# Performance work log

Hardware: AMD Instinct MI355X
Metric: run time of the kernel (lower is better)

The kernel has to match this reference:

```python
import jax, jax.numpy as jnp
import numpy as np

DIM = 256
TIME_DIM = 64
BETA = 0.5
VOCAB = 150
B, L = 2048, 128


def setup_inputs() -> dict:
    key = jax.random.key(0)
    ks = jax.random.split(key, 9)
    u = lambda k, shape: jax.random.uniform(k, shape, jnp.float32, -0.1, 0.1)
    return {
        "out": jax.random.normal(ks[0], (B, L, DIM), jnp.float32),
        "hn": jax.random.normal(ks[1], (B, DIM), jnp.float32),
        "pos_ind": jax.random.randint(ks[2], (B, L), 0, VOCAB),
        "rel_dt": jax.random.randint(ks[3], (B, L), 0, VOCAB),
        "abs_dt": jnp.zeros((B, L), jnp.float32),
        "pos_emb_w": u(ks[4], (VOCAB, TIME_DIM)),
        "rel_emb_w": u(ks[5], (VOCAB, TIME_DIM)),
        "Wk": u(ks[6], (DIM, DIM)),   # fc_k.weight: y = x @ Wk.T
        "Wq": u(ks[7], (DIM, DIM)),   # fc_q.weight
        "Wrp": u(ks[8], (1, 2 * TIME_DIM)),  # fc_rp.weight
    }


def reference(out, hn, pos_ind, rel_dt, abs_dt, pos_emb_w, rel_emb_w, Wk, Wq, Wrp):
    temperature = np.sqrt(DIM * 1.0).astype(np.float32)
    pad_mask = pos_ind == 0                      # [B, L]
    pos_e = pos_emb_w[pos_ind]                   # [B, L, T]
    rel_e = rel_emb_w[rel_dt]                    # [B, L, T]
    attn_k = jnp.einsum('bld,ed->ble', out, Wk)  # fc_k(out)
    attn_q = jnp.einsum('bd,ed->be', hn, Wq)     # fc_q(hn)
    attn_0 = jnp.einsum('bld,bd->bl', attn_k, attn_q) / temperature
    attn_1 = jnp.einsum('blt,ot->bl', jnp.concatenate([rel_e, pos_e], -1), Wrp)
    attn = attn_0 + BETA * attn_1
    attn = jnp.where(pad_mask, -jnp.inf, attn)
    attn = jax.nn.softmax(attn, axis=1)
    return jnp.einsum('bl,bld->bd', attn, out)   # [B, D]
```

## Files before the change

kernel.cpp:

```cpp
#include <hip/hip_runtime.h>

#define DIM 256
#define L_ 128
#define TD 64
#define NVOCAB 150
#define NB 2048

__device__ __forceinline__ float dot4(float4 a, float4 b) {
    return fmaf(a.x, b.x, fmaf(a.y, b.y, fmaf(a.z, b.z, a.w * b.w)));
}

__global__ __launch_bounds__(256) void prep_kernel(
    const float* __restrict__ Wk, const float* __restrict__ Wq,
    const float* __restrict__ Wrp,
    const float* __restrict__ rel_emb_w, const float* __restrict__ pos_emb_w,
    float* __restrict__ M, float* __restrict__ rel_s, float* __restrict__ pos_s)
{
    if (blockIdx.x == DIM) {
        int v = threadIdx.x;
        if (v < NVOCAB) {
            float sr = 0.f, sp = 0.f;
#pragma unroll 8
            for (int j = 0; j < TD; ++j) {
                sr = fmaf(rel_emb_w[v * TD + j], Wrp[j], sr);
                sp = fmaf(pos_emb_w[v * TD + j], Wrp[TD + j], sp);
            }
            rel_s[v] = 0.5f * sr;
            pos_s[v] = 0.5f * sp;
        }
        return;
    }
    int cc = blockIdx.x;
    int d  = threadIdx.x;
    float a0 = 0.f, a1 = 0.f, a2 = 0.f, a3 = 0.f;
#pragma unroll 8
    for (int e = 0; e < DIM; e += 4) {
        a0 = fmaf(Wq[(e + 0) * DIM + cc], Wk[(e + 0) * DIM + d], a0);
        a1 = fmaf(Wq[(e + 1) * DIM + cc], Wk[(e + 1) * DIM + d], a1);
        a2 = fmaf(Wq[(e + 2) * DIM + cc], Wk[(e + 2) * DIM + d], a2);
        a3 = fmaf(Wq[(e + 3) * DIM + cc], Wk[(e + 3) * DIM + d], a3);
    }
    M[cc * DIM + d] = (a0 + a1 + a2 + a3) * (1.0f / 16.0f);
}

__global__ __launch_bounds__(256) void qk_bias_kernel(
    const float* __restrict__ hn, const float* __restrict__ M,
    const int* __restrict__ pos_ind, const int* __restrict__ rel_dt,
    const float* __restrict__ rel_s, const float* __restrict__ pos_s,
    float* __restrict__ qk, float* __restrict__ bias_g)
{
    const int t = threadIdx.x;
    if (blockIdx.x >= NB / 8) {
        int idx = (blockIdx.x - NB / 8) * 256 + t;
        int pi = pos_ind[idx];
        int rd = rel_dt[idx];
        bias_g[idx] = (pi == 0) ? -1e30f : (rel_s[rd] + pos_s[pi]);
        return;
    }
    __shared__ float hn_s[8][DIM];
    const int r0 = blockIdx.x * 8;
#pragma unroll
    for (int i = 0; i < 8; ++i)
        hn_s[i][t] = hn[(size_t)(r0 + i) * DIM + t];
    __syncthreads();
    float acc[8] = {0.f, 0.f, 0.f, 0.f, 0.f, 0.f, 0.f, 0.f};
#pragma unroll 8
    for (int c = 0; c < DIM; ++c) {
        float m = M[c * DIM + t];
#pragma unroll
        for (int r = 0; r < 8; ++r)
            acc[r] = fmaf(hn_s[r][c], m, acc[r]);
    }
#pragma unroll
    for (int r = 0; r < 8; ++r)
        qk[(size_t)(r0 + r) * DIM + t] = acc[r];
}

__global__ __launch_bounds__(256) void attn_wave(
    const float* __restrict__ outp, const float* __restrict__ qk,
    const float* __restrict__ bias_g, float* __restrict__ y)
{
    const int w    = threadIdx.x >> 6;
    const int lane = threadIdx.x & 63;
    const int g    = lane >> 4;
    const int c    = lane & 15;
    const int b    = (blockIdx.x << 2) | w;

    const float4* __restrict__ src = (const float4*)outp + (size_t)b * (L_ * 64);
    const float4* __restrict__ qp  = (const float4*)qk + (size_t)b * 64;
    const float*  __restrict__ bp  = bias_g + (size_t)b * L_;

    float4 q[4];
#pragma unroll
    for (int j = 0; j < 4; ++j) q[j] = qp[j * 16 + c];

    float4 o[4];
#pragma unroll
    for (int j = 0; j < 4; ++j) o[j] = make_float4(0.f, 0.f, 0.f, 0.f);
    float d = 0.f;

    float4 va[4], vb[4];
    float biA, biB;

#define LOADV(BUF, ROW)                                            \
    do {                                                           \
        _Pragma("unroll")                                          \
        for (int j = 0; j < 4; ++j)                                \
            BUF[j] = src[(ROW) * 64 + j * 16 + c];                 \
    } while (0)

#define PROC(BUF, BI)                                              \
    do {                                                           \
        float p = dot4(BUF[0], q[0]) + dot4(BUF[1], q[1]) +        \
                  dot4(BUF[2], q[2]) + dot4(BUF[3], q[3]);         \
        p += __shfl_xor(p, 1);                                     \
        p += __shfl_xor(p, 2);                                     \
        p += __shfl_xor(p, 4);                                     \
        p += __shfl_xor(p, 8);                                     \
        float we = __expf(p + (BI));                               \
        d += we;                                                   \
        _Pragma("unroll")                                          \
        for (int j = 0; j < 4; ++j) {                              \
            o[j].x = fmaf(we, BUF[j].x, o[j].x);                   \
            o[j].y = fmaf(we, BUF[j].y, o[j].y);                   \
            o[j].z = fmaf(we, BUF[j].z, o[j].z);                   \
            o[j].w = fmaf(we, BUF[j].w, o[j].w);                   \
        }                                                          \
    } while (0)

    LOADV(va, g);         biA = bp[g];
    LOADV(vb, 4 + g);     biB = bp[4 + g];

    for (int rb = 0; rb < L_ - 8; rb += 8) {
        PROC(va, biA);
        LOADV(va, rb + 8 + g);   biA = bp[rb + 8 + g];
        PROC(vb, biB);
        LOADV(vb, rb + 12 + g);  biB = bp[rb + 12 + g];
    }
    PROC(va, biA);
    PROC(vb, biB);
#undef LOADV
#undef PROC

#pragma unroll
    for (int j = 0; j < 4; ++j) {
        o[j].x += __shfl_xor(o[j].x, 16); o[j].y += __shfl_xor(o[j].y, 16);
        o[j].z += __shfl_xor(o[j].z, 16); o[j].w += __shfl_xor(o[j].w, 16);
        o[j].x += __shfl_xor(o[j].x, 32); o[j].y += __shfl_xor(o[j].y, 32);
        o[j].z += __shfl_xor(o[j].z, 32); o[j].w += __shfl_xor(o[j].w, 32);
    }
    d += __shfl_xor(d, 16);
    d += __shfl_xor(d, 32);

    const float inv = 1.0f / d;
    if (lane < 16) {
        float4* __restrict__ yo = (float4*)(y + (size_t)b * DIM);
#pragma unroll
        for (int j = 0; j < 4; ++j)
            yo[j * 16 + c] = make_float4(o[j].x * inv, o[j].y * inv,
                                         o[j].z * inv, o[j].w * inv);
    }
}

extern "C" void kernel_launch(void* const* d_in, const int* in_sizes, int n_in,
                              void* d_out, int out_size, void* d_ws, size_t ws_size,
                              hipStream_t stream)
{
    const float* out_t     = (const float*)d_in[0];
    const float* hn        = (const float*)d_in[1];
    const int*   pos_ind   = (const int*)  d_in[2];
    const int*   rel_dt    = (const int*)  d_in[3];
    const float* pos_emb_w = (const float*)d_in[5];
    const float* rel_emb_w = (const float*)d_in[6];
    const float* Wk        = (const float*)d_in[7];
    const float* Wq        = (const float*)d_in[8];
    const float* Wrp       = (const float*)d_in[9];

    float* y = (float*)d_out;

    float* M      = (float*)d_ws;
    float* qk     = M + DIM * DIM;
    float* rel_s  = qk + (size_t)NB * DIM;
    float* pos_s  = rel_s + 256;
    float* bias_g = pos_s + 256;

    prep_kernel<<<DIM + 1, 256, 0, stream>>>(Wk, Wq, Wrp, rel_emb_w, pos_emb_w,
                                             M, rel_s, pos_s);
    qk_bias_kernel<<<NB / 8 + (NB * L_) / 256, 256, 0, stream>>>(
        hn, M, pos_ind, rel_dt, rel_s, pos_s, qk, bias_g);
    attn_wave<<<NB / 4, 256, 0, stream>>>(out_t, qk, bias_g, y);
}
```

Measured before the change: 81.98 us.

## Fuse weight prep, query projection, bias lookup and attention into one kernel

The three launches are replaced by a single kernel that handles 4 batch rows per block. Each block computes the vocab score tables in shared memory, projects hn through Wq and then Wk to get the effective query, and looks up the bias on the fly from pos_ind and rel_dt. This removes two launches and the global round trips for M, qk and bias_g. In exchange every one of the 512 blocks rereads all of Wq and Wk (256 KB each, mostly from cache) and recomputes the embedding tables, which is redundant work ahead of the bandwidth-bound streaming of `out`. The first rows of `out` are loaded before this preamble so their latency overlaps it.

```diff
diff --git a/kernel.cpp b/kernel.cpp
--- a/kernel.cpp
+++ b/kernel.cpp
@@ -10,135 +10,156 @@
     return fmaf(a.x, b.x, fmaf(a.y, b.y, fmaf(a.z, b.z, a.w * b.w)));
 }
 
-__global__ __launch_bounds__(256) void prep_kernel(
+__global__ __launch_bounds__(256) void fused_kernel(
+    const float* __restrict__ outp, const float* __restrict__ hn,
+    const int* __restrict__ pos_ind, const int* __restrict__ rel_dt,
+    const float* __restrict__ pos_emb_w, const float* __restrict__ rel_emb_w,
     const float* __restrict__ Wk, const float* __restrict__ Wq,
-    const float* __restrict__ Wrp,
-    const float* __restrict__ rel_emb_w, const float* __restrict__ pos_emb_w,
-    float* __restrict__ M, float* __restrict__ rel_s, float* __restrict__ pos_s)
+    const float* __restrict__ Wrp, float* __restrict__ y)
 {
-    if (blockIdx.x == DIM) {
-        int v = threadIdx.x;
-        if (v < NVOCAB) {
-            float sr = 0.f, sp = 0.f;
-#pragma unroll 8
-            for (int j = 0; j < TD; ++j) {
-                sr = fmaf(rel_emb_w[v * TD + j], Wrp[j], sr);
-                sp = fmaf(pos_emb_w[v * TD + j], Wrp[TD + j], sp);
-            }
-            rel_s[v] = 0.5f * sr;
-            pos_s[v] = 0.5f * sp;
-        }
-        return;
-    }
-    int cc = blockIdx.x;
-    int d  = threadIdx.x;
-    float a0 = 0.f, a1 = 0.f, a2 = 0.f, a3 = 0.f;
-#pragma unroll 8
-    for (int e = 0; e < DIM; e += 4) {
-        a0 = fmaf(Wq[(e + 0) * DIM + cc], Wk[(e + 0) * DIM + d], a0);
-        a1 = fmaf(Wq[(e + 1) * DIM + cc], Wk[(e + 1) * DIM + d], a1);
-        a2 = fmaf(Wq[(e + 2) * DIM + cc], Wk[(e + 2) * DIM + d], a2);
-        a3 = fmaf(Wq[(e + 3) * DIM + cc], Wk[(e + 3) * DIM + d], a3);
-    }
-    M[cc * DIM + d] = (a0 + a1 + a2 + a3) * (1.0f / 16.0f);
-}
-
-__global__ __launch_bounds__(256) void qk_bias_kernel(
-    const float* __restrict__ hn, const float* __restrict__ M,
-    const int* __restrict__ pos_ind, const int* __restrict__ rel_dt,
-    const float* __restrict__ rel_s, const float* __restrict__ pos_s,
-    float* __restrict__ qk, float* __restrict__ bias_g)
-{
-    const int t = threadIdx.x;
-    if (blockIdx.x >= NB / 8) {
-        int idx = (blockIdx.x - NB / 8) * 256 + t;
-        int pi = pos_ind[idx];
-        int rd = rel_dt[idx];
-        bias_g[idx] = (pi == 0) ? -1e30f : (rel_s[rd] + pos_s[pi]);
-        return;
-    }
-    __shared__ float hn_s[8][DIM];
-    const int r0 = blockIdx.x * 8;
-#pragma unroll
-    for (int i = 0; i < 8; ++i)
-        hn_s[i][t] = hn[(size_t)(r0 + i) * DIM + t];
-    __syncthreads();
-    float acc[8] = {0.f, 0.f, 0.f, 0.f, 0.f, 0.f, 0.f, 0.f};
-#pragma unroll 8
-    for (int c = 0; c < DIM; ++c) {
-        float m = M[c * DIM + t];
-#pragma unroll
-        for (int r = 0; r < 8; ++r)
-            acc[r] = fmaf(hn_s[r][c], m, acc[r]);
-    }
-#pragma unroll
-    for (int r = 0; r < 8; ++r)
-        qk[(size_t)(r0 + r) * DIM + t] = acc[r];
-}
-
-__global__ __launch_bounds__(256) void attn_wave(
-    const float* __restrict__ outp, const float* __restrict__ qk,
-    const float* __restrict__ bias_g, float* __restrict__ y)
-{
-    const int w    = threadIdx.x >> 6;
-    const int lane = threadIdx.x & 63;
+    const int t  = threadIdx.x;
+    const int b0 = blockIdx.x << 2;
+
+    const int w    = t >> 6;
+    const int lane = t & 63;
     const int g    = lane >> 4;
     const int c    = lane & 15;
-    const int b    = (blockIdx.x << 2) | w;
+    const int b    = b0 + w;
+
+    __shared__ float hn_s[4][DIM];
+    __shared__ float aq_s[4][DIM];
+    __shared__ float qk_s[4][DIM];
+    __shared__ float rel_s[NVOCAB];
+    __shared__ float pos_s[NVOCAB];
 
     const float4* __restrict__ src = (const float4*)outp + (size_t)b * (L_ * 64);
-    const float4* __restrict__ qp  = (const float4*)qk + (size_t)b * 64;
-    const float*  __restrict__ bp  = bias_g + (size_t)b * L_;
+    const int*    __restrict__ pip = pos_ind + (size_t)b * L_;
+    const int*    __restrict__ rdp = rel_dt  + (size_t)b * L_;
+
+    float4 va[4], vb[4];
+    int piA, rdA, piB, rdB;
+#pragma unroll
+    for (int j = 0; j < 4; ++j) va[j] = src[g * 64 + j * 16 + c];
+#pragma unroll
+    for (int j = 0; j < 4; ++j) vb[j] = src[(4 + g) * 64 + j * 16 + c];
+    piA = pip[g];     rdA = rdp[g];
+    piB = pip[4 + g]; rdB = rdp[4 + g];
+
+#pragma unroll
+    for (int i = 0; i < 4; ++i)
+        hn_s[i][t] = hn[(size_t)(b0 + i) * DIM + t];
+    if (t < NVOCAB) {
+        float sr = 0.f, sp = 0.f;
+#pragma unroll 8
+        for (int j = 0; j < TD; ++j) {
+            sr = fmaf(rel_emb_w[t * TD + j], Wrp[j], sr);
+            sp = fmaf(pos_emb_w[t * TD + j], Wrp[TD + j], sp);
+        }
+        rel_s[t] = 0.5f * sr;
+        pos_s[t] = 0.5f * sp;
+    }
+    __syncthreads();
+
+    {
+        const int G = t >> 4;
+        const float4* __restrict__ hn4 = (const float4*)hn_s;
+        float4 hf[4][4];
+#pragma unroll
+        for (int bb = 0; bb < 4; ++bb)
+#pragma unroll
+            for (int j = 0; j < 4; ++j)
+                hf[bb][j] = hn4[bb * 64 + j * 16 + c];
+        const float4* __restrict__ Wq4 = (const float4*)Wq;
+        for (int k = 0; k < 16; ++k) {
+            const int e = (G << 4) + k;
+            float4 wq[4];
+#pragma unroll
+            for (int j = 0; j < 4; ++j)
+                wq[j] = Wq4[e * 64 + j * 16 + c];
+#pragma unroll
+            for (int bb = 0; bb < 4; ++bb) {
+                float p = dot4(wq[0], hf[bb][0]) + dot4(wq[1], hf[bb][1])
+                        + dot4(wq[2], hf[bb][2]) + dot4(wq[3], hf[bb][3]);
+                p += __shfl_xor(p, 1);
+                p += __shfl_xor(p, 2);
+                p += __shfl_xor(p, 4);
+                p += __shfl_xor(p, 8);
+                if (c == bb) aq_s[bb][e] = p * 0.0625f;
+            }
+        }
+    }
+    __syncthreads();
+
+    {
+        const int b2 = t >> 6, d4 = t & 63;
+        const float4* __restrict__ Wk4 = (const float4*)Wk;
+        const float4* __restrict__ aq4 = (const float4*)aq_s[b2];
+        float4 acc = make_float4(0.f, 0.f, 0.f, 0.f);
+        for (int e4 = 0; e4 < 64; ++e4) {
+            const float4 a4 = aq4[e4];
+            const float4 wk0 = Wk4[(e4 * 4 + 0) * 64 + d4];
+            const float4 wk1 = Wk4[(e4 * 4 + 1) * 64 + d4];
+            const float4 wk2 = Wk4[(e4 * 4 + 2) * 64 + d4];
+            const float4 wk3 = Wk4[(e4 * 4 + 3) * 64 + d4];
+            acc.x = fmaf(a4.x, wk0.x, acc.x); acc.y = fmaf(a4.x, wk0.y, acc.y);
+            acc.z = fmaf(a4.x, wk0.z, acc.z); acc.w = fmaf(a4.x, wk0.w, acc.w);
+            acc.x = fmaf(a4.y, wk1.x, acc.x); acc.y = fmaf(a4.y, wk1.y, acc.y);
+            acc.z = fmaf(a4.y, wk1.z, acc.z); acc.w = fmaf(a4.y, wk1.w, acc.w);
+            acc.x = fmaf(a4.z, wk2.x, acc.x); acc.y = fmaf(a4.z, wk2.y, acc.y);
+            acc.z = fmaf(a4.z, wk2.z, acc.z); acc.w = fmaf(a4.z, wk2.w, acc.w);
+            acc.x = fmaf(a4.w, wk3.x, acc.x); acc.y = fmaf(a4.w, wk3.y, acc.y);
+            acc.z = fmaf(a4.w, wk3.z, acc.z); acc.w = fmaf(a4.w, wk3.w, acc.w);
+        }
+        ((float4*)qk_s[b2])[d4] = acc;
+    }
+    __syncthreads();
 
     float4 q[4];
 #pragma unroll
-    for (int j = 0; j < 4; ++j) q[j] = qp[j * 16 + c];
+    for (int j = 0; j < 4; ++j) q[j] = ((const float4*)qk_s[w])[j * 16 + c];
 
     float4 o[4];
 #pragma unroll
     for (int j = 0; j < 4; ++j) o[j] = make_float4(0.f, 0.f, 0.f, 0.f);
     float d = 0.f;
 
-    float4 va[4], vb[4];
-    float biA, biB;
-
-#define LOADV(BUF, ROW)                                            \
-    do {                                                           \
-        _Pragma("unroll")                                          \
-        for (int j = 0; j < 4; ++j)                                \
-            BUF[j] = src[(ROW) * 64 + j * 16 + c];                 \
+#define LOADV(BUF, ROW)                                           \
+    do { _Pragma("unroll")                                        \
+        for (int j = 0; j < 4; ++j)                               \
+            BUF[j] = src[(ROW) * 64 + j * 16 + c];                \
     } while (0)
 
-#define PROC(BUF, BI)                                              \
-    do {                                                           \
-        float p = dot4(BUF[0], q[0]) + dot4(BUF[1], q[1]) +        \
-                  dot4(BUF[2], q[2]) + dot4(BUF[3], q[3]);         \
-        p += __shfl_xor(p, 1);                                     \
-        p += __shfl_xor(p, 2);                                     \
-        p += __shfl_xor(p, 4);                                     \
-        p += __shfl_xor(p, 8);                                     \
-        float we = __expf(p + (BI));                               \
-        d += we;                                                   \
-        _Pragma("unroll")                                          \
-        for (int j = 0; j < 4; ++j) {                              \
-            o[j].x = fmaf(we, BUF[j].x, o[j].x);                   \
-            o[j].y = fmaf(we, BUF[j].y, o[j].y);                   \
-            o[j].z = fmaf(we, BUF[j].z, o[j].z);                   \
-            o[j].w = fmaf(we, BUF[j].w, o[j].w);                   \
-        }                                                          \
+#define PROC(BUF, PI, RD)                                         \
+    do {                                                          \
+        float p = dot4(BUF[0], q[0]) + dot4(BUF[1], q[1]) +       \
+                  dot4(BUF[2], q[2]) + dot4(BUF[3], q[3]);        \
+        p += __shfl_xor(p, 1);                                    \
+        p += __shfl_xor(p, 2);                                    \
+        p += __shfl_xor(p, 4);                                    \
+        p += __shfl_xor(p, 8);                                    \
+        float bi = ((PI) == 0) ? -1e30f                           \
+                 : rel_s[(RD)] + pos_s[(PI)];                     \
+        float we = __expf(p + bi);                                \
+        d += we;                                                  \
+        _Pragma("unroll")                                         \
+        for (int j = 0; j < 4; ++j) {                             \
+            o[j].x = fmaf(we, BUF[j].x, o[j].x);                  \
+            o[j].y = fmaf(we, BUF[j].y, o[j].y);                  \
+            o[j].z = fmaf(we, BUF[j].z, o[j].z);                  \
+            o[j].w = fmaf(we, BUF[j].w, o[j].w);                  \
+        }                                                         \
     } while (0)
 
-    LOADV(va, g);         biA = bp[g];
-    LOADV(vb, 4 + g);     biB = bp[4 + g];
-
     for (int rb = 0; rb < L_ - 8; rb += 8) {
-        PROC(va, biA);
-        LOADV(va, rb + 8 + g);   biA = bp[rb + 8 + g];
-        PROC(vb, biB);
-        LOADV(vb, rb + 12 + g);  biB = bp[rb + 12 + g];
-    }
-    PROC(va, biA);
-    PROC(vb, biB);
+        PROC(va, piA, rdA);
+        LOADV(va, rb + 8 + g);
+        piA = pip[rb + 8 + g];  rdA = rdp[rb + 8 + g];
+        PROC(vb, piB, rdB);
+        LOADV(vb, rb + 12 + g);
+        piB = pip[rb + 12 + g]; rdB = rdp[rb + 12 + g];
+    }
+    PROC(va, piA, rdA);
+    PROC(vb, piB, rdB);
 #undef LOADV
 #undef PROC
 
@@ -178,15 +199,6 @@
 
     float* y = (float*)d_out;
 
-    float* M      = (float*)d_ws;
-    float* qk     = M + DIM * DIM;
-    float* rel_s  = qk + (size_t)NB * DIM;
-    float* pos_s  = rel_s + 256;
-    float* bias_g = pos_s + 256;
-
-    prep_kernel<<<DIM + 1, 256, 0, stream>>>(Wk, Wq, Wrp, rel_emb_w, pos_emb_w,
-                                             M, rel_s, pos_s);
-    qk_bias_kernel<<<NB / 8 + (NB * L_) / 256, 256, 0, stream>>>(
-        hn, M, pos_ind, rel_dt, rel_s, pos_s, qk, bias_g);
-    attn_wave<<<NB / 4, 256, 0, stream>>>(out_t, qk, bias_g, y);
+    fused_kernel<<<NB / 4, 256, 0, stream>>>(
+        out_t, hn, pos_ind, rel_dt, pos_emb_w, rel_emb_w, Wk, Wq, Wrp, y);
 }
```

Measured after the change: 81.28 us. About the same (-0.9%).
